# Optimization experiments

Measured on AMD Instinct MI355X. Metric: run time of the kernel, lower is better.

## Reference

```python
import jax, jax.numpy as jnp
import numpy as np

EMB = 1024
HEADS = 16
HEAD_DIM = EMB // HEADS

def setup_inputs() -> dict:
    key = jax.random.key(0)
    ks = jax.random.split(key, 12)
    s = 0.02
    x = jax.random.normal(ks[0], (2, 2048, EMB), dtype=jnp.float32)
    return {
        "x": x,
        "wq": jax.random.normal(ks[1], (EMB, EMB), jnp.float32) * s,
        "bq": jnp.zeros((EMB,), jnp.float32),
        "wk": jax.random.normal(ks[2], (EMB, EMB), jnp.float32) * s,
        "bk": jnp.zeros((EMB,), jnp.float32),
        "wv": jax.random.normal(ks[3], (EMB, EMB), jnp.float32) * s,
        "bv": jnp.zeros((EMB,), jnp.float32),
        "wo": jax.random.normal(ks[4], (EMB, EMB), jnp.float32) * s,
        "bo": jnp.zeros((EMB,), jnp.float32),
        "gamma": jnp.ones((EMB,), jnp.float32),
        "beta": jnp.zeros((EMB,), jnp.float32),
    }

def _layernorm(x, gamma, beta, eps=1e-5):
    mu = jnp.mean(x, axis=-1, keepdims=True)
    var = jnp.mean(jnp.square(x - mu), axis=-1, keepdims=True)
    return (x - mu) * jax.lax.rsqrt(var + eps) * gamma + beta

def reference(x, wq, bq, wk, bk, wv, bv, wo, bo, gamma, beta):
    B, T, D = x.shape
    H, d_k = HEADS, HEAD_DIM
    # Linear(y = x W^T + b), then split heads
    q = (x @ wq.T + bq).reshape(B, T, H, d_k)
    k = (x @ wk.T + bk).reshape(B, T, H, d_k)
    v = (x @ wv.T + bv).reshape(B, T, H, d_k)
    scores = jnp.einsum('bthd,bshd->bhts', q, k) / jnp.sqrt(jnp.float32(d_k))
    attn = jax.nn.softmax(scores, axis=-1)  # dropout is identity in eval mode
    out = jnp.einsum('bhts,bshd->bthd', attn, v).reshape(B, T, D)
    out = out @ wo.T + bo
    return _layernorm(x + out, gamma, beta)
```

## Files before the change

### kernel.cpp

```cpp
#include <hip/hip_runtime.h>
#include <stdint.h>
#include <stddef.h>


typedef __bf16 bf16_t;
typedef bf16_t bf16x8 __attribute__((ext_vector_type(8)));
typedef float f32x16 __attribute__((ext_vector_type(16)));
typedef float f32x2 __attribute__((ext_vector_type(2)));
typedef uint16_t u16x8 __attribute__((ext_vector_type(8)));

#define MFMA32(a, b, c) __builtin_amdgcn_mfma_f32_32x32x16_bf16((a), (b), (c), 0, 0, 0)

__device__ __forceinline__ uint16_t f2bf(float f) {
  __bf16 h = (__bf16)f;
  return *(uint16_t*)&h;
}

__device__ __forceinline__ void gload16(const void* g, void* l) {
  __builtin_amdgcn_global_load_lds((const __attribute__((address_space(1))) void*)g,
                                   (__attribute__((address_space(3))) void*)l,
                                   16, 0, 0);
}

__global__ __launch_bounds__(256) void cvt_all(
    const float* __restrict__ x, const float* __restrict__ wq,
    const float* __restrict__ wk, const float* __restrict__ wv,
    const float* __restrict__ wo, uint16_t* __restrict__ xb,
    uint16_t* __restrict__ wqb, uint16_t* __restrict__ wkb,
    uint16_t* __restrict__ wvb, uint16_t* __restrict__ wob) {
  const int gid = blockIdx.x * 256 + threadIdx.x;
  const float* src; uint16_t* dst; int off;
  if (gid < 1048576) {
    src = x; dst = xb; off = gid;
  } else {
    const int t = gid - 1048576;
    off = t & 262143;
    switch (t >> 18) {
      case 0: src = wq; dst = wqb; break;
      case 1: src = wk; dst = wkb; break;
      case 2: src = wv; dst = wvb; break;
      default: src = wo; dst = wob; break;
    }
  }
  const float4 f = ((const float4*)src)[off];
  uint64_t p = (uint64_t)f2bf(f.x) | ((uint64_t)f2bf(f.y) << 16) |
               ((uint64_t)f2bf(f.z) << 32) | ((uint64_t)f2bf(f.w) << 48);
  ((uint64_t*)dst)[off] = p;
}

template <bool OUT_BF16>
__device__ __forceinline__ void gemm128(const uint16_t* __restrict__ A,
                                        const uint16_t* __restrict__ Bt,
                                        const float* __restrict__ bias,
                                        float oscale,
                                        uint16_t* __restrict__ outb,
                                        float* __restrict__ outf) {
  __shared__ uint16_t sA[2][128 * 32];
  __shared__ uint16_t sB[2][128 * 32];
  const int tid = threadIdx.x;
  const int lane = tid & 63, w = tid >> 6;
  const int l31 = lane & 31, half = lane >> 5;
  const int m0 = blockIdx.y * 128, n0 = blockIdx.x * 128;
  const int wm = (w >> 1) * 64, wn = (w & 1) * 64;

  const int ch0 = tid, ch1 = tid + 256;
  const int r0 = ch0 >> 2, g0 = (((ch0 & 3) ^ (r0 & 3)) << 3);
  const int r1 = ch1 >> 2, g1 = (((ch1 & 3) ^ (r1 & 3)) << 3);
  const uint16_t* a0 = A + (size_t)(m0 + r0) * 1024 + g0;
  const uint16_t* a1 = A + (size_t)(m0 + r1) * 1024 + g1;
  const uint16_t* b0 = Bt + (size_t)(n0 + r0) * 1024 + g0;
  const uint16_t* b1 = Bt + (size_t)(n0 + r1) * 1024 + g1;

  gload16(a0, &sA[0][ch0 * 8]);
  gload16(a1, &sA[0][ch1 * 8]);
  gload16(b0, &sB[0][ch0 * 8]);
  gload16(b1, &sB[0][ch1 * 8]);

  f32x16 acc[2][2] = {};

  for (int kt = 0; kt < 32; ++kt) {
    __syncthreads();
    const int cur = kt & 1;
    if (kt < 31) {
      const int ko = (kt + 1) * 32;
      const int nxt = cur ^ 1;
      gload16(a0 + ko, &sA[nxt][ch0 * 8]);
      gload16(a1 + ko, &sA[nxt][ch1 * 8]);
      gload16(b0 + ko, &sB[nxt][ch0 * 8]);
      gload16(b1 + ko, &sB[nxt][ch1 * 8]);
    }
#pragma unroll
    for (int s = 0; s < 2; ++s) {
      const int c = s * 2 + half;
      bf16x8 af[2], bfr[2];
#pragma unroll
      for (int i = 0; i < 2; ++i) {
        const int arow = wm + i * 32 + l31;
        af[i] = *(const bf16x8*)&sA[cur][arow * 32 + ((c ^ (arow & 3)) << 3)];
      }
#pragma unroll
      for (int j = 0; j < 2; ++j) {
        const int brow = wn + j * 32 + l31;
        bfr[j] = *(const bf16x8*)&sB[cur][brow * 32 + ((c ^ (brow & 3)) << 3)];
      }
#pragma unroll
      for (int i = 0; i < 2; ++i)
#pragma unroll
        for (int j = 0; j < 2; ++j) acc[i][j] = MFMA32(af[i], bfr[j], acc[i][j]);
    }
  }

#pragma unroll
  for (int i = 0; i < 2; ++i) {
#pragma unroll
    for (int j = 0; j < 2; ++j) {
      const int gn = n0 + wn + j * 32 + l31;
      const float bv = bias[gn];
#pragma unroll
      for (int reg = 0; reg < 16; ++reg) {
        const int gm = m0 + wm + i * 32 + (reg & 3) + 8 * (reg >> 2) + 4 * half;
        const float v = (acc[i][j][reg] + bv) * oscale;
        const size_t idx = (size_t)gm * 1024 + gn;
        if constexpr (OUT_BF16) outb[idx] = f2bf(v);
        else outf[idx] = v;
      }
    }
  }
}

#define QSCALE 0.18033688011112042f

__global__ __launch_bounds__(256) void qkv_gemm(
    const uint16_t* __restrict__ xb, const uint16_t* __restrict__ wqb,
    const uint16_t* __restrict__ wkb, const uint16_t* __restrict__ wvb,
    const float* __restrict__ bq, const float* __restrict__ bk,
    const float* __restrict__ bv, uint16_t* __restrict__ qb,
    uint16_t* __restrict__ kb, uint16_t* __restrict__ vb) {
  const uint16_t* Bt; const float* bias; uint16_t* out; float sc;
  if (blockIdx.z == 0)      { Bt = wqb; bias = bq; out = qb; sc = QSCALE; }
  else if (blockIdx.z == 1) { Bt = wkb; bias = bk; out = kb; sc = 1.f; }
  else                      { Bt = wvb; bias = bv; out = vb; sc = 1.f; }
  gemm128<true>(xb, Bt, bias, sc, out, nullptr);
}

__global__ __launch_bounds__(256) void o_gemm(const uint16_t* __restrict__ ab,
                                              const uint16_t* __restrict__ wob,
                                              const float* __restrict__ bo,
                                              float* __restrict__ y) {
  gemm128<false>(ab, wob, bo, 1.f, nullptr, y);
}

__global__ __launch_bounds__(256) void v_trans(const uint16_t* __restrict__ vb,
                                               uint16_t* __restrict__ vbT) {
  __shared__ uint16_t sT[64 * 136];
  const int tid = threadIdx.x;
  const int t0 = blockIdx.x * 128;
  const int h = blockIdx.y, b = blockIdx.z;
#pragma unroll
  for (int c = 0; c < 4; ++c) {
    const int idx = c * 256 + tid;
    const int t = idx >> 3, d8 = (idx & 7) * 8;
    u16x8 v = *(const u16x8*)&vb[(size_t)(b * 2048 + t0 + t) * 1024 + h * 64 + d8];
#pragma unroll
    for (int e = 0; e < 8; ++e) sT[(d8 + e) * 136 + t] = v[e];
  }
  __syncthreads();
  const size_t obase = ((size_t)(b * 16 + h) * 64) * 2048 + t0;
#pragma unroll
  for (int c = 0; c < 4; ++c) {
    const int idx = c * 256 + tid;
    const int d = idx >> 4, t8 = (idx & 15) * 8;
    const int tb = t8 & ~15;
    const int add4 = (t8 & 8) ? 4 : 0;
    u16x8 v;
#pragma unroll
    for (int e = 0; e < 8; ++e)
      v[e] = sT[d * 136 + tb + ((e & 3) + ((e >> 2) << 3)) + add4];
    *(u16x8*)&vbT[obase + (size_t)d * 2048 + t8] = v;
  }
}


#define QK_CHUNK(accv, mblk_)                                               \
  do {                                                                      \
    const int srow_ = sh * 64 + (mblk_) * 32 + l31;                         \
    _Pragma("unroll") for (int s4_ = 0; s4_ < 4; ++s4_) {                   \
      const int c_ = s4_ * 2 + half;                                        \
      const bf16x8 kk_ =                                                    \
          *(const bf16x8*)&sKc[srow_ * 64 + ((c_ ^ (srow_ & 7)) << 3)];     \
      accv = MFMA32(kk_, qa[s4_], accv);                                    \
    }                                                                       \
  } while (0)

#define EXP_PACK(accv, b0_, b1_)                                            \
  do {                                                                      \
    _Pragma("unroll") for (int r_ = 0; r_ < 8; r_ += 2) {                   \
      const float pa_ = __builtin_amdgcn_exp2f(accv[r_]);                   \
      const float pb_ = __builtin_amdgcn_exp2f(accv[r_ + 1]);               \
      li2 += (f32x2){pa_, pb_};                                             \
      b0_[r_] = (__bf16)pa_;                                                \
      b0_[r_ + 1] = (__bf16)pb_;                                            \
    }                                                                       \
    _Pragma("unroll") for (int r_ = 0; r_ < 8; r_ += 2) {                   \
      const float pa_ = __builtin_amdgcn_exp2f(accv[r_ + 8]);               \
      const float pb_ = __builtin_amdgcn_exp2f(accv[r_ + 9]);               \
      li2 += (f32x2){pa_, pb_};                                             \
      b1_[r_] = (__bf16)pa_;                                                \
      b1_[r_ + 1] = (__bf16)pb_;                                            \
    }                                                                       \
  } while (0)

#define PV_CHUNK(mblk_, b0_, b1_)                                           \
  do {                                                                      \
    _Pragma("unroll") for (int t_ = 0; t_ < 2; ++t_) {                      \
      const bf16x8 bp_ = t_ ? (b1_) : (b0_);                                \
      const int cc_ = sh * 8 + (mblk_) * 4 + t_ * 2 + half;                 \
      _Pragma("unroll") for (int md_ = 0; md_ < 2; ++md_) {                 \
        const int vrow_ = md_ * 32 + l31;                                   \
        const bf16x8 vv_ =                                                  \
            *(const bf16x8*)&sVc[vrow_ * 128 + ((cc_ ^ (vrow_ & 15)) << 3)];\
        acc_o[md_] = MFMA32(vv_, bp_, acc_o[md_]);                          \
      }                                                                     \
    }                                                                       \
  } while (0)

__global__ __launch_bounds__(512, 4) void attn(const uint16_t* __restrict__ qb,
                                               const uint16_t* __restrict__ kb,
                                               const uint16_t* __restrict__ vbT,
                                               uint16_t* __restrict__ ab) {
  __shared__ __align__(16) uint16_t smem[32768];
  uint16_t* sK = smem;
  uint16_t* sV = smem + 16384;
  const int tid = threadIdx.x;
  const int lane = tid & 63, w = tid >> 6;
  const int l31 = lane & 31, half = lane >> 5;
  const int rg = w & 3, sh = w >> 2;
  const int hb = blockIdx.x;
  const int h = hb & 15, b = hb >> 4;
  const int q0 = blockIdx.y * 128;
  const size_t qkbase = (size_t)b * 2048 * 1024 + (size_t)h * 64;
  const size_t vtbase = (size_t)hb * 64 * 2048;

  const int ch0 = tid, ch1 = tid + 512;
  const int kr0 = ch0 >> 3, kg0 = (((ch0 & 7) ^ (kr0 & 7)) << 3);
  const int kr1 = ch1 >> 3, kg1 = (((ch1 & 7) ^ (kr1 & 7)) << 3);
  const int vr0 = ch0 >> 4, vg0 = (((ch0 & 15) ^ (vr0 & 15)) << 3);
  const int vr1 = ch1 >> 4, vg1 = (((ch1 & 15) ^ (vr1 & 15)) << 3);
  const uint16_t* k0 = kb + qkbase + (size_t)kr0 * 1024 + kg0;
  const uint16_t* k1 = kb + qkbase + (size_t)kr1 * 1024 + kg1;
  const uint16_t* v0 = vbT + vtbase + (size_t)vr0 * 2048 + vg0;
  const uint16_t* v1 = vbT + vtbase + (size_t)vr1 * 2048 + vg1;

  gload16(k0, sK + ch0 * 8);
  gload16(k1, sK + ch1 * 8);
  gload16(v0, sV + ch0 * 8);
  gload16(v1, sV + ch1 * 8);

  bf16x8 qa[4];
  {
    const uint16_t* qrow =
        qb + qkbase + (size_t)(q0 + rg * 32 + l31) * 1024 + half * 8;
#pragma unroll
    for (int s4 = 0; s4 < 4; ++s4) qa[s4] = *(const bf16x8*)(qrow + s4 * 16);
  }

  f32x16 acc_o[2] = {};
  f32x2 li2 = {0.f, 0.f};

  for (int kt = 0; kt < 16; ++kt) {
    __syncthreads();
    const int cur = kt & 1;
    if (kt < 15) {
      const size_t soK = (size_t)(kt + 1) * 128 * 1024;
      const int soV = (kt + 1) * 128;
      const int nxt = cur ^ 1;
      gload16(k0 + soK, sK + nxt * 8192 + ch0 * 8);
      gload16(k1 + soK, sK + nxt * 8192 + ch1 * 8);
      gload16(v0 + soV, sV + nxt * 8192 + ch0 * 8);
      gload16(v1 + soV, sV + nxt * 8192 + ch1 * 8);
    }
    const uint16_t* sKc = sK + cur * 8192;
    const uint16_t* sVc = sV + cur * 8192;

    f32x16 acc0 = {}, acc1 = {};
    __builtin_amdgcn_s_setprio(1);
    QK_CHUNK(acc0, 0);
    QK_CHUNK(acc1, 1);
    __builtin_amdgcn_s_setprio(0);

    bf16x8 p00, p01, p10, p11;
    EXP_PACK(acc0, p00, p01);
    __builtin_amdgcn_s_setprio(1);
    PV_CHUNK(0, p00, p01);
    __builtin_amdgcn_s_setprio(0);
    EXP_PACK(acc1, p10, p11);
    __builtin_amdgcn_s_setprio(1);
    PV_CHUNK(1, p10, p11);
    __builtin_amdgcn_s_setprio(0);
  }

  float li = li2.x + li2.y;

  __syncthreads();
  float* ep = (float*)smem;
  float* epl = (float*)(smem + 16384);
  if (sh == 1) {
#pragma unroll
    for (int md = 0; md < 2; ++md)
#pragma unroll
      for (int reg = 0; reg < 16; ++reg)
        ep[((rg * 2 + md) * 16 + reg) * 64 + lane] = acc_o[md][reg];
    epl[rg * 64 + lane] = li;
  }
  __syncthreads();
  if (sh == 0) {
#pragma unroll
    for (int md = 0; md < 2; ++md)
#pragma unroll
      for (int reg = 0; reg < 16; ++reg)
        acc_o[md][reg] += ep[((rg * 2 + md) * 16 + reg) * 64 + lane];
    li += epl[rg * 64 + lane];
    li += __shfl_xor(li, 32);
    const float inv = 1.f / li;
    const int row = q0 + rg * 32 + l31;
    uint16_t* const obase = ab + (size_t)(b * 2048 + row) * 1024 + h * 64;
#pragma unroll
    for (int md = 0; md < 2; ++md)
#pragma unroll
      for (int g = 0; g < 4; ++g) {
        uint64_t pk = 0;
#pragma unroll
        for (int e = 0; e < 4; ++e)
          pk |= (uint64_t)f2bf(acc_o[md][g * 4 + e] * inv) << (16 * e);
        *(uint64_t*)(obase + md * 32 + g * 8 + half * 4) = pk;
      }
  }
}

__global__ __launch_bounds__(256) void resid_ln(const float* __restrict__ x,
                                                const float* __restrict__ y,
                                                const float* __restrict__ gamma,
                                                const float* __restrict__ beta,
                                                float* __restrict__ out) {
  const int row = blockIdx.x, tid = threadIdx.x;
  const size_t base = (size_t)row * 1024 + tid * 4;
  const float4 xv = *(const float4*)(x + base);
  const float4 yv = *(const float4*)(y + base);
  const float a = xv.x + yv.x, b2 = xv.y + yv.y, c = xv.z + yv.z, d = xv.w + yv.w;
  float s = a + b2 + c + d;
#pragma unroll
  for (int o = 1; o < 64; o <<= 1) s += __shfl_xor(s, o);
  __shared__ float red[4];
  const int w = tid >> 6;
  if ((tid & 63) == 0) red[w] = s;
  __syncthreads();
  const float mu = (red[0] + red[1] + red[2] + red[3]) * (1.f / 1024.f);
  const float da = a - mu, db = b2 - mu, dc = c - mu, dd = d - mu;
  float sq = da * da + db * db + dc * dc + dd * dd;
#pragma unroll
  for (int o = 1; o < 64; o <<= 1) sq += __shfl_xor(sq, o);
  __syncthreads();
  if ((tid & 63) == 0) red[w] = sq;
  __syncthreads();
  const float var = (red[0] + red[1] + red[2] + red[3]) * (1.f / 1024.f);
  const float rs = rsqrtf(var + 1e-5f);
  const float4 g = *(const float4*)(gamma + tid * 4);
  const float4 bt = *(const float4*)(beta + tid * 4);
  float4 o4;
  o4.x = da * rs * g.x + bt.x;
  o4.y = db * rs * g.y + bt.y;
  o4.z = dc * rs * g.z + bt.z;
  o4.w = dd * rs * g.w + bt.w;
  *(float4*)(out + base) = o4;
}

extern "C" void kernel_launch(void* const* d_in, const int* in_sizes, int n_in,
                              void* d_out, int out_size, void* d_ws, size_t ws_size,
                              hipStream_t stream) {
  const float* x     = (const float*)d_in[0];
  const float* wq    = (const float*)d_in[1];
  const float* bq    = (const float*)d_in[2];
  const float* wk    = (const float*)d_in[3];
  const float* bk    = (const float*)d_in[4];
  const float* wv    = (const float*)d_in[5];
  const float* bv    = (const float*)d_in[6];
  const float* wo    = (const float*)d_in[7];
  const float* bo    = (const float*)d_in[8];
  const float* gamma = (const float*)d_in[9];
  const float* beta  = (const float*)d_in[10];
  float* out = (float*)d_out;
  char* ws = (char*)d_ws;
  const size_t MB = 1024 * 1024;
  uint16_t* xb  = (uint16_t*)(ws);
  uint16_t* ab  = xb;
  uint16_t* wqb = (uint16_t*)(ws + 8 * MB);
  uint16_t* wkb = (uint16_t*)(ws + 10 * MB);
  uint16_t* wvb = (uint16_t*)(ws + 12 * MB);
  uint16_t* wob = (uint16_t*)(ws + 14 * MB);
  uint16_t* qb  = (uint16_t*)(ws + 16 * MB);
  uint16_t* kb  = (uint16_t*)(ws + 24 * MB);
  uint16_t* vb  = (uint16_t*)(ws + 32 * MB);
  uint16_t* vbT = (uint16_t*)(ws + 40 * MB);
  float*    y   = (float*)(ws + 16 * MB);

  cvt_all<<<8192, 256, 0, stream>>>(x, wq, wk, wv, wo, xb, wqb, wkb, wvb, wob);
  qkv_gemm<<<dim3(8, 32, 3), 256, 0, stream>>>(xb, wqb, wkb, wvb, bq, bk, bv, qb, kb, vb);
  v_trans<<<dim3(16, 16, 2), 256, 0, stream>>>(vb, vbT);
  attn<<<dim3(32, 16), 512, 0, stream>>>(qb, kb, vbT, ab);
  o_gemm<<<dim3(8, 32), 256, 0, stream>>>(ab, wob, bo, y);
  resid_ln<<<4096, 256, 0, stream>>>(x, y, gamma, beta, out);
}
```

Measured before the change: 208.6 us.

## Use 64x128 tiles for output GEMM and serialize QK/PV chunks in attention

Adds a dedicated 64x128-tile GEMM for the output projection and launches twice as many blocks, so more of the GPU's compute units get work on the M=4096,N=1024 problem. The attention inner loop also changes: it now runs the QK, exp and PV steps for one chunk before starting the next, and drops the s_setprio hints. This lowers register pressure (one score accumulator live instead of two), but it gives up the interleaving that let the exp work of one chunk hide behind MFMA work. The smaller GEMM tiles mean more global and LDS traffic per FLOP.

```diff
diff --git a/kernel.cpp b/kernel.cpp
--- a/kernel.cpp
+++ b/kernel.cpp
@@ -128,6 +128,71 @@
   }
 }
 
+__device__ __forceinline__ void gemm64x128(const uint16_t* __restrict__ A,
+                                           const uint16_t* __restrict__ Bt,
+                                           const float* __restrict__ bias,
+                                           float* __restrict__ outf) {
+  __shared__ uint16_t sA[2][64 * 32];
+  __shared__ uint16_t sB[2][128 * 32];
+  const int tid = threadIdx.x;
+  const int lane = tid & 63, w = tid >> 6;
+  const int l31 = lane & 31, half = lane >> 5;
+  const int m0 = blockIdx.y * 64, n0 = blockIdx.x * 128;
+  const int wm = (w >> 1) * 32, wn = (w & 1) * 64;
+
+  const int ra = tid >> 2, ga = (((tid & 3) ^ (ra & 3)) << 3);
+  const int chb0 = tid, chb1 = tid + 256;
+  const int rb0 = chb0 >> 2, gb0 = (((chb0 & 3) ^ (rb0 & 3)) << 3);
+  const int rb1 = chb1 >> 2, gb1 = (((chb1 & 3) ^ (rb1 & 3)) << 3);
+  const uint16_t* a0 = A + (size_t)(m0 + ra) * 1024 + ga;
+  const uint16_t* b0 = Bt + (size_t)(n0 + rb0) * 1024 + gb0;
+  const uint16_t* b1 = Bt + (size_t)(n0 + rb1) * 1024 + gb1;
+
+  gload16(a0, &sA[0][tid * 8]);
+  gload16(b0, &sB[0][chb0 * 8]);
+  gload16(b1, &sB[0][chb1 * 8]);
+
+  f32x16 acc[2] = {};
+
+  for (int kt = 0; kt < 32; ++kt) {
+    __syncthreads();
+    const int cur = kt & 1;
+    if (kt < 31) {
+      const int ko = (kt + 1) * 32;
+      const int nxt = cur ^ 1;
+      gload16(a0 + ko, &sA[nxt][tid * 8]);
+      gload16(b0 + ko, &sB[nxt][chb0 * 8]);
+      gload16(b1 + ko, &sB[nxt][chb1 * 8]);
+    }
+#pragma unroll
+    for (int s = 0; s < 2; ++s) {
+      const int c = s * 2 + half;
+      const int arow = wm + l31;
+      const bf16x8 af =
+          *(const bf16x8*)&sA[cur][arow * 32 + ((c ^ (arow & 3)) << 3)];
+      bf16x8 bfr[2];
+#pragma unroll
+      for (int j = 0; j < 2; ++j) {
+        const int brow = wn + j * 32 + l31;
+        bfr[j] = *(const bf16x8*)&sB[cur][brow * 32 + ((c ^ (brow & 3)) << 3)];
+      }
+#pragma unroll
+      for (int j = 0; j < 2; ++j) acc[j] = MFMA32(af, bfr[j], acc[j]);
+    }
+  }
+
+#pragma unroll
+  for (int j = 0; j < 2; ++j) {
+    const int gn = n0 + wn + j * 32 + l31;
+    const float bv = bias[gn];
+#pragma unroll
+    for (int reg = 0; reg < 16; ++reg) {
+      const int gm = m0 + wm + (reg & 3) + 8 * (reg >> 2) + 4 * half;
+      outf[(size_t)gm * 1024 + gn] = acc[j][reg] + bv;
+    }
+  }
+}
+
 #define QSCALE 0.18033688011112042f
 
 __global__ __launch_bounds__(256) void qkv_gemm(
@@ -147,7 +212,7 @@
                                               const uint16_t* __restrict__ wob,
                                               const float* __restrict__ bo,
                                               float* __restrict__ y) {
-  gemm128<false>(ab, wob, bo, 1.f, nullptr, y);
+  gemm64x128(ab, wob, bo, y);
 }
 
 __global__ __launch_bounds__(256) void v_trans(const uint16_t* __restrict__ vb,
@@ -282,21 +347,14 @@
     const uint16_t* sKc = sK + cur * 8192;
     const uint16_t* sVc = sV + cur * 8192;
 
-    f32x16 acc0 = {}, acc1 = {};
-    __builtin_amdgcn_s_setprio(1);
-    QK_CHUNK(acc0, 0);
-    QK_CHUNK(acc1, 1);
-    __builtin_amdgcn_s_setprio(0);
-
-    bf16x8 p00, p01, p10, p11;
-    EXP_PACK(acc0, p00, p01);
-    __builtin_amdgcn_s_setprio(1);
-    PV_CHUNK(0, p00, p01);
-    __builtin_amdgcn_s_setprio(0);
-    EXP_PACK(acc1, p10, p11);
-    __builtin_amdgcn_s_setprio(1);
-    PV_CHUNK(1, p10, p11);
-    __builtin_amdgcn_s_setprio(0);
+#pragma unroll
+    for (int mblk = 0; mblk < 2; ++mblk) {
+      f32x16 accs = {};
+      QK_CHUNK(accs, mblk);
+      bf16x8 bp0, bp1;
+      EXP_PACK(accs, bp0, bp1);
+      PV_CHUNK(mblk, bp0, bp1);
+    }
   }
 
   float li = li2.x + li2.y;
@@ -407,6 +465,6 @@
   qkv_gemm<<<dim3(8, 32, 3), 256, 0, stream>>>(xb, wqb, wkb, wvb, bq, bk, bv, qb, kb, vb);
   v_trans<<<dim3(16, 16, 2), 256, 0, stream>>>(vb, vbT);
   attn<<<dim3(32, 16), 512, 0, stream>>>(qb, kb, vbT, ab);
-  o_gemm<<<dim3(8, 32), 256, 0, stream>>>(ab, wob, bo, y);
+  o_gemm<<<dim3(8, 64), 256, 0, stream>>>(ab, wob, bo, y);
   resid_ln<<<4096, 256, 0, stream>>>(x, y, gamma, beta, out);
 }
```

After: 207.9 us. About the same (-0.4%).
